# Kernel optimization log

Measured on AMD Instinct MI355X. Metric: run time of the kernel, lower is better.

The kernel has to match this reference:

```python
import jax, jax.numpy as jnp
import numpy as np

B, P, H, W = 64, 2, 512, 512

def setup_inputs() -> dict:
    key = jax.random.key(0)
    k1, k2 = jax.random.split(key)
    inp = jax.random.normal(k1, (B, P, H, W), dtype=jnp.float32)
    tgt = jax.random.uniform(k2, (B, P, H, W), dtype=jnp.float32)
    return {"input": inp, "target": tgt}


def reference(input, target):
    b, p, h, w = input.shape  # p == 2 required by the original loss
    # DSNT soft-argmax: softmax over flattened heatmap, expectation over grids
    sm = jax.nn.softmax(input.reshape(b, p, h * w), axis=-1).reshape(b, p, h, w)
    x_grid = (jnp.arange(1, w + 1, dtype=input.dtype)) / w  # [W]
    y_grid = (jnp.arange(1, h + 1, dtype=input.dtype)) / h  # [H]
    pred_x = jnp.einsum('bphw,w->bp', sm, x_grid)
    pred_y = jnp.einsum('bphw,h->bp', sm, y_grid)
    # ground-truth argmax coords (detached / non-differentiable)
    am = jnp.argmax(target.reshape(b, p, h * w), axis=-1)  # [B,P]
    true_x = ((am % w).astype(input.dtype) + 1.0) / w
    true_y = ((am // w).astype(input.dtype) + 1.0) / h
    # euclidean distance loss per (sample, point)
    ed = jnp.sqrt((true_x - pred_x) ** 2 + (true_y - pred_y) ** 2)  # [B,P]
    s = jnp.sum(ed)
    # vector between point 0 and point 1 (x, y) per sample
    pred_vec = jnp.stack([pred_x[:, 0] - pred_x[:, 1], pred_y[:, 0] - pred_y[:, 1]], axis=-1)  # [B,2]
    true_vec = jnp.stack([true_x[:, 0] - true_x[:, 1], true_y[:, 0] - true_y[:, 1]], axis=-1)  # [B,2]
    pred_dist = jnp.sqrt(jnp.sum(pred_vec ** 2, axis=-1))  # [B]
    true_dist = jnp.sqrt(jnp.sum(true_vec ** 2, axis=-1))  # [B]
    s = s + jnp.sum(jnp.sqrt((pred_dist - true_dist) ** 2))
    # NOTE: original applies cos() to the cosine similarity (faithful reproduction)
    dot = jnp.sum(pred_vec * true_vec, axis=-1)  # [B]
    cos_distance = 1.0 - jnp.cos(dot / (pred_dist * true_dist))
    s = s + jnp.sum(cos_distance)
    return jnp.reshape(s / b, (1,))
```

## Files before the change

### kernel.cpp

```cpp
#include <hip/hip_runtime.h>
#include <math.h>

#define HH 512
#define WW 512
#define BP 128
#define SEG 16
#define PLANE (HH * WW)
#define SEG_ELEMS (PLANE / SEG)
#define NPART (BP * SEG)


__global__ __launch_bounds__(256) void dsnt_partial(
    const float* __restrict__ inp, const float* __restrict__ tgt,
    float* __restrict__ wsf, int* __restrict__ wsi)
{
    const int blk  = blockIdx.x;
    const int pair = blk >> 4;
    const int seg  = blk & 15;
    const int tid  = threadIdx.x;

    const size_t base = (size_t)pair * PLANE + (size_t)seg * SEG_ELEMS;
    const float4* __restrict__ ip = (const float4*)(inp + base);
    const float4* __restrict__ tp = (const float4*)(tgt + base);

    const float inv = 1.0f / 512.0f;
    const int segbase = seg * SEG_ELEMS;

    float s = 0.0f, sx = 0.0f, sy = 0.0f;
    float mv = -1.0f;
    int   mi = 0;

#pragma unroll
    for (int o = 0; o < 4; ++o) {
        float4 a[4], bb[4];
#pragma unroll
        for (int j = 0; j < 4; ++j) a[j]  = ip[o * 1024 + j * 256 + tid];
#pragma unroll
        for (int j = 0; j < 4; ++j) bb[j] = tp[o * 1024 + j * 256 + tid];

#pragma unroll
        for (int j = 0; j < 4; ++j) {
            const int vidx = o * 1024 + j * 256 + tid;
            const int f = segbase + vidx * 4;
            const float yw  = (float)((f >> 9) + 1) * inv;
            const float xw0 = (float)((f & 511) + 1) * inv;

            const float e0 = __expf(a[j].x);
            const float e1 = __expf(a[j].y);
            const float e2 = __expf(a[j].z);
            const float e3 = __expf(a[j].w);
            const float es = e0 + e1 + e2 + e3;
            s  += es;
            sx += es * xw0 + inv * (e1 + 2.0f * e2 + 3.0f * e3);
            sy += es * yw;

            if (bb[j].x > mv) { mv = bb[j].x; mi = f; }
            if (bb[j].y > mv) { mv = bb[j].y; mi = f + 1; }
            if (bb[j].z > mv) { mv = bb[j].z; mi = f + 2; }
            if (bb[j].w > mv) { mv = bb[j].w; mi = f + 3; }
        }
    }

#pragma unroll
    for (int off = 32; off > 0; off >>= 1) {
        s  += __shfl_down(s,  off, 64);
        sx += __shfl_down(sx, off, 64);
        sy += __shfl_down(sy, off, 64);
        const float ov = __shfl_down(mv, off, 64);
        const int   oi = __shfl_down(mi, off, 64);
        if (ov > mv || (ov == mv && oi < mi)) { mv = ov; mi = oi; }
    }

    __shared__ float rs[4], rsx[4], rsy[4], rmv[4];
    __shared__ int   rmi[4];
    const int lane = tid & 63, wid = tid >> 6;
    if (lane == 0) { rs[wid] = s; rsx[wid] = sx; rsy[wid] = sy; rmv[wid] = mv; rmi[wid] = mi; }
    __syncthreads();
    if (tid == 0) {
        float fs = rs[0], fsx = rsx[0], fsy = rsy[0], fmv = rmv[0];
        int fmi = rmi[0];
#pragma unroll
        for (int k = 1; k < 4; ++k) {
            fs += rs[k]; fsx += rsx[k]; fsy += rsy[k];
            if (rmv[k] > fmv || (rmv[k] == fmv && rmi[k] < fmi)) { fmv = rmv[k]; fmi = rmi[k]; }
        }
        wsf[blk]             = fs;
        wsf[NPART + blk]     = fsx;
        wsf[2 * NPART + blk] = fsy;
        wsf[3 * NPART + blk] = fmv;
        wsi[blk]             = fmi;
    }
}

__global__ __launch_bounds__(128) void dsnt_finalize(
    const float* __restrict__ wsf, const int* __restrict__ wsi,
    float* __restrict__ out)
{
    __shared__ float px[BP], py[BP], tx[BP], ty[BP];
    __shared__ float wsum[2];
    const int tid = threadIdx.x;

    {
        float s = 0.0f, sx = 0.0f, sy = 0.0f, mv = -1.0f;
        int mi = 0;
#pragma unroll
        for (int k = 0; k < SEG; ++k) {
            const int i = tid * SEG + k;
            s  += wsf[i];
            sx += wsf[NPART + i];
            sy += wsf[2 * NPART + i];
            const float v = wsf[3 * NPART + i];
            const int  ii = wsi[i];
            if (v > mv || (v == mv && ii < mi)) { mv = v; mi = ii; }
        }
        px[tid] = sx / s;
        py[tid] = sy / s;
        tx[tid] = (float)((mi & 511) + 1) * (1.0f / 512.0f);
        ty[tid] = (float)((mi >> 9) + 1) * (1.0f / 512.0f);
    }
    __syncthreads();

    float term = 0.0f;
    if (tid < 64) {
        const int b = tid;
        const float px0 = px[2 * b], px1 = px[2 * b + 1];
        const float py0 = py[2 * b], py1 = py[2 * b + 1];
        const float tx0 = tx[2 * b], tx1 = tx[2 * b + 1];
        const float ty0 = ty[2 * b], ty1 = ty[2 * b + 1];

        const float ed0 = sqrtf((tx0 - px0) * (tx0 - px0) + (ty0 - py0) * (ty0 - py0));
        const float ed1 = sqrtf((tx1 - px1) * (tx1 - px1) + (ty1 - py1) * (ty1 - py1));

        const float pvx = px0 - px1, pvy = py0 - py1;
        const float tvx = tx0 - tx1, tvy = ty0 - ty1;
        const float pd = sqrtf(pvx * pvx + pvy * pvy);
        const float td = sqrtf(tvx * tvx + tvy * tvy);
        const float dot = pvx * tvx + pvy * tvy;
        const float cosd = 1.0f - cosf(dot / (pd * td));
        term = ed0 + ed1 + fabsf(pd - td) + cosd;
    }

#pragma unroll
    for (int off = 32; off > 0; off >>= 1)
        term += __shfl_down(term, off, 64);
    const int lane = tid & 63, wid = tid >> 6;
    if (lane == 0) wsum[wid] = term;
    __syncthreads();
    if (tid == 0) out[0] = (wsum[0] + wsum[1]) * (1.0f / 64.0f);
}

extern "C" void kernel_launch(void* const* d_in, const int* in_sizes, int n_in,
                              void* d_out, int out_size, void* d_ws, size_t ws_size,
                              hipStream_t stream)
{
    const float* inp = (const float*)d_in[0];
    const float* tgt = (const float*)d_in[1];
    float* out = (float*)d_out;
    float* wsf = (float*)d_ws;
    int*   wsi = (int*)((float*)d_ws + 4 * NPART);

    dsnt_partial<<<NPART, 256, 0, stream>>>(inp, tgt, wsf, wsi);
    dsnt_finalize<<<1, 128, 0, stream>>>(wsf, wsi, out);
}
```

Measured before the change: 280.0 us.

## Split softmax-moment and argmax work into separate block groups with finer segments

```diff
diff --git a/kernel.cpp b/kernel.cpp
--- a/kernel.cpp
+++ b/kernel.cpp
@@ -4,91 +4,111 @@
 #define HH 512
 #define WW 512
 #define BP 128
-#define SEG 16
 #define PLANE (HH * WW)
-#define SEG_ELEMS (PLANE / SEG)
-#define NPART (BP * SEG)
+#define SEG2 32
+#define SEG2_F4 2048
+#define NPART2 (BP * SEG2)
 
 
 __global__ __launch_bounds__(256) void dsnt_partial(
     const float* __restrict__ inp, const float* __restrict__ tgt,
     float* __restrict__ wsf, int* __restrict__ wsi)
 {
+    const int tid  = threadIdx.x;
     const int blk  = blockIdx.x;
-    const int pair = blk >> 4;
-    const int seg  = blk & 15;
-    const int tid  = threadIdx.x;
-
-    const size_t base = (size_t)pair * PLANE + (size_t)seg * SEG_ELEMS;
-    const float4* __restrict__ ip = (const float4*)(inp + base);
-    const float4* __restrict__ tp = (const float4*)(tgt + base);
-
+    const int lane = tid & 63, wid = tid >> 6;
     const float inv = 1.0f / 512.0f;
-    const int segbase = seg * SEG_ELEMS;
-
-    float s = 0.0f, sx = 0.0f, sy = 0.0f;
-    float mv = -1.0f;
-    int   mi = 0;
-
-#pragma unroll
-    for (int o = 0; o < 4; ++o) {
-        float4 a[4], bb[4];
-#pragma unroll
-        for (int j = 0; j < 4; ++j) a[j]  = ip[o * 1024 + j * 256 + tid];
-#pragma unroll
-        for (int j = 0; j < 4; ++j) bb[j] = tp[o * 1024 + j * 256 + tid];
-
-#pragma unroll
-        for (int j = 0; j < 4; ++j) {
-            const int vidx = o * 1024 + j * 256 + tid;
-            const int f = segbase + vidx * 4;
-            const float yw  = (float)((f >> 9) + 1) * inv;
-            const float xw0 = (float)((f & 511) + 1) * inv;
-
-            const float e0 = __expf(a[j].x);
-            const float e1 = __expf(a[j].y);
-            const float e2 = __expf(a[j].z);
-            const float e3 = __expf(a[j].w);
-            const float es = e0 + e1 + e2 + e3;
-            s  += es;
-            sx += es * xw0 + inv * (e1 + 2.0f * e2 + 3.0f * e3);
-            sy += es * yw;
-
-            if (bb[j].x > mv) { mv = bb[j].x; mi = f; }
-            if (bb[j].y > mv) { mv = bb[j].y; mi = f + 1; }
-            if (bb[j].z > mv) { mv = bb[j].z; mi = f + 2; }
-            if (bb[j].w > mv) { mv = bb[j].w; mi = f + 3; }
-        }
-    }
-
-#pragma unroll
-    for (int off = 32; off > 0; off >>= 1) {
-        s  += __shfl_down(s,  off, 64);
-        sx += __shfl_down(sx, off, 64);
-        sy += __shfl_down(sy, off, 64);
-        const float ov = __shfl_down(mv, off, 64);
-        const int   oi = __shfl_down(mi, off, 64);
-        if (ov > mv || (ov == mv && oi < mi)) { mv = ov; mi = oi; }
-    }
 
     __shared__ float rs[4], rsx[4], rsy[4], rmv[4];
     __shared__ int   rmi[4];
-    const int lane = tid & 63, wid = tid >> 6;
-    if (lane == 0) { rs[wid] = s; rsx[wid] = sx; rsy[wid] = sy; rmv[wid] = mv; rmi[wid] = mi; }
-    __syncthreads();
-    if (tid == 0) {
-        float fs = rs[0], fsx = rsx[0], fsy = rsy[0], fmv = rmv[0];
-        int fmi = rmi[0];
+
+    if (blk < NPART2) {
+        const int pair = blk >> 5;
+        const int seg  = blk & 31;
+        const float4* __restrict__ ip =
+            (const float4*)(inp + (size_t)pair * PLANE) + seg * SEG2_F4;
+        const int segbase = seg * (SEG2_F4 * 4);
+
+        float s = 0.0f, sx = 0.0f, sy = 0.0f;
 #pragma unroll
-        for (int k = 1; k < 4; ++k) {
-            fs += rs[k]; fsx += rsx[k]; fsy += rsy[k];
-            if (rmv[k] > fmv || (rmv[k] == fmv && rmi[k] < fmi)) { fmv = rmv[k]; fmi = rmi[k]; }
+        for (int o = 0; o < 2; ++o) {
+            float4 a[4];
+#pragma unroll
+            for (int j = 0; j < 4; ++j) a[j] = ip[(o * 4 + j) * 256 + tid];
+#pragma unroll
+            for (int j = 0; j < 4; ++j) {
+                const int f = segbase + ((o * 4 + j) * 256 + tid) * 4;
+                const float yw  = (float)((f >> 9) + 1) * inv;
+                const float xw0 = (float)((f & 511) + 1) * inv;
+                const float e0 = __expf(a[j].x);
+                const float e1 = __expf(a[j].y);
+                const float e2 = __expf(a[j].z);
+                const float e3 = __expf(a[j].w);
+                const float es = e0 + e1 + e2 + e3;
+                s  += es;
+                sx += es * xw0 + inv * (e1 + 2.0f * e2 + 3.0f * e3);
+                sy += es * yw;
+            }
         }
-        wsf[blk]             = fs;
-        wsf[NPART + blk]     = fsx;
-        wsf[2 * NPART + blk] = fsy;
-        wsf[3 * NPART + blk] = fmv;
-        wsi[blk]             = fmi;
+
+#pragma unroll
+        for (int off = 32; off > 0; off >>= 1) {
+            s  += __shfl_down(s,  off, 64);
+            sx += __shfl_down(sx, off, 64);
+            sy += __shfl_down(sy, off, 64);
+        }
+        if (lane == 0) { rs[wid] = s; rsx[wid] = sx; rsy[wid] = sy; }
+        __syncthreads();
+        if (tid == 0) {
+            float fs = rs[0], fsx = rsx[0], fsy = rsy[0];
+#pragma unroll
+            for (int k = 1; k < 4; ++k) { fs += rs[k]; fsx += rsx[k]; fsy += rsy[k]; }
+            wsf[blk]              = fs;
+            wsf[NPART2 + blk]     = fsx;
+            wsf[2 * NPART2 + blk] = fsy;
+        }
+    } else {
+        const int b2   = blk - NPART2;
+        const int pair = b2 >> 5;
+        const int seg  = b2 & 31;
+        const float4* __restrict__ tp =
+            (const float4*)(tgt + (size_t)pair * PLANE) + seg * SEG2_F4;
+        const int segbase = seg * (SEG2_F4 * 4);
+
+        float mv = -1.0f;
+        int   mi = 0;
+#pragma unroll
+        for (int o = 0; o < 2; ++o) {
+            float4 bb[4];
+#pragma unroll
+            for (int j = 0; j < 4; ++j) bb[j] = tp[(o * 4 + j) * 256 + tid];
+#pragma unroll
+            for (int j = 0; j < 4; ++j) {
+                const int f = segbase + ((o * 4 + j) * 256 + tid) * 4;
+                if (bb[j].x > mv) { mv = bb[j].x; mi = f; }
+                if (bb[j].y > mv) { mv = bb[j].y; mi = f + 1; }
+                if (bb[j].z > mv) { mv = bb[j].z; mi = f + 2; }
+                if (bb[j].w > mv) { mv = bb[j].w; mi = f + 3; }
+            }
+        }
+
+#pragma unroll
+        for (int off = 32; off > 0; off >>= 1) {
+            const float ov = __shfl_down(mv, off, 64);
+            const int   oi = __shfl_down(mi, off, 64);
+            if (ov > mv || (ov == mv && oi < mi)) { mv = ov; mi = oi; }
+        }
+        if (lane == 0) { rmv[wid] = mv; rmi[wid] = mi; }
+        __syncthreads();
+        if (tid == 0) {
+            float fmv = rmv[0];
+            int   fmi = rmi[0];
+#pragma unroll
+            for (int k = 1; k < 4; ++k)
+                if (rmv[k] > fmv || (rmv[k] == fmv && rmi[k] < fmi)) { fmv = rmv[k]; fmi = rmi[k]; }
+            wsf[3 * NPART2 + b2] = fmv;
+            wsi[b2]              = fmi;
+        }
     }
 }
 
@@ -104,12 +124,12 @@
         float s = 0.0f, sx = 0.0f, sy = 0.0f, mv = -1.0f;
         int mi = 0;
 #pragma unroll
-        for (int k = 0; k < SEG; ++k) {
-            const int i = tid * SEG + k;
+        for (int k = 0; k < SEG2; ++k) {
+            const int i = tid * SEG2 + k;
             s  += wsf[i];
-            sx += wsf[NPART + i];
-            sy += wsf[2 * NPART + i];
-            const float v = wsf[3 * NPART + i];
+            sx += wsf[NPART2 + i];
+            sy += wsf[2 * NPART2 + i];
+            const float v = wsf[3 * NPART2 + i];
             const int  ii = wsi[i];
             if (v > mv || (v == mv && ii < mi)) { mv = v; mi = ii; }
         }
@@ -157,8 +177,8 @@
     const float* tgt = (const float*)d_in[1];
     float* out = (float*)d_out;
     float* wsf = (float*)d_ws;
-    int*   wsi = (int*)((float*)d_ws + 4 * NPART);
+    int*   wsi = (int*)((float*)d_ws + 4 * NPART2);
 
-    dsnt_partial<<<NPART, 256, 0, stream>>>(inp, tgt, wsf, wsi);
+    dsnt_partial<<<2 * NPART2, 256, 0, stream>>>(inp, tgt, wsf, wsi);
     dsnt_finalize<<<1, 128, 0, stream>>>(wsf, wsi, out);
 }
```

After: 281.6 us. Within noise of the previous version (+0.6%).
